# Performance work log

Measured on AMD Instinct MI355X. Metric: run time of the kernel, lower is better.

The kernel has to match this reference:

```python
import jax, jax.numpy as jnp
import numpy as np

NUM_CLASS = 20
STRIDE = 4.0
B, H, W, G, NV = 8, 128, 128, 64, 40


def setup_inputs() -> dict:
    key = jax.random.key(0)
    ks = jax.random.split(key, 8)
    keypoints = jax.random.normal(ks[0], (B, H, W, NUM_CLASS), jnp.float32)
    preg = jax.random.uniform(ks[1], (B, H, W, 4), jnp.float32, 1.0, 40.0)
    fpn = jax.random.normal(ks[2], (B, H, W, NUM_CLASS), jnp.float32)
    masks = jnp.ones((B, H, W, G), jnp.float32)
    scalar_y = jax.random.uniform(ks[3], (B, G), jnp.float32, 5.0, 25.0)
    scalar_x = jax.random.uniform(ks[4], (B, G), jnp.float32, 5.0, 25.0)
    # ground truth: [cy, cx, y1, x1, y2, x2, class]; rows >= NV are zero padding
    rng = np.random.default_rng(0)
    gt = np.zeros((B, G, 7), np.float32)
    cy = rng.uniform(20.0, 492.0, (B, NV)).astype(np.float32)
    cx = rng.uniform(20.0, 492.0, (B, NV)).astype(np.float32)
    hh = rng.uniform(16.0, 120.0, (B, NV)).astype(np.float32)
    ww = rng.uniform(16.0, 120.0, (B, NV)).astype(np.float32)
    gt[:, :NV, 0] = cy
    gt[:, :NV, 1] = cx
    gt[:, :NV, 2] = np.clip(cy - hh / 2, 1.0, 510.0)
    gt[:, :NV, 3] = np.clip(cx - ww / 2, 1.0, 510.0)
    gt[:, :NV, 4] = np.clip(cy + hh / 2, 1.0, 510.0)
    gt[:, :NV, 5] = np.clip(cx + ww / 2, 1.0, 510.0)
    gt[:, :NV, 6] = rng.integers(1, NUM_CLASS + 1, (B, NV)).astype(np.float32)
    return {
        "keypoints": keypoints,
        "preg": preg,
        "fpn": fpn,
        "ground_truth": jnp.asarray(gt),
        "masks": masks,
        "scalar_y": scalar_y,
        "scalar_x": scalar_x,
    }


def _image_loss(gravity_pred, dist_pred, heatmap_pred, gt, masks, sy, sx):
    f32 = jnp.float32
    Hh, Ww, C = gravity_pred.shape
    Gg = gt.shape[0]
    # padding boundary: first row whose cy (col 0) is the minimum (==0 padding)
    slice_index = jnp.argmin(gt[:, 0])
    valid = jnp.arange(Gg) < slice_index
    vf = valid.astype(f32)

    gy = (gt[:, 0] + 0.5) / STRIDE
    gx = (gt[:, 1] + 0.5) / STRIDE
    by1 = (gt[:, 2] + 0.5) / STRIDE
    bx1 = (gt[:, 3] + 0.5) / STRIDE
    by2 = (gt[:, 4] + 0.5) / STRIDE
    bx2 = (gt[:, 5] + 0.5) / STRIDE
    cid = gt[:, 6].astype(jnp.int32) - 1
    kp_y = jnp.clip(jnp.floor(gt[:, 0] / STRIDE).astype(jnp.int32), 0, Hh - 1)
    kp_x = jnp.clip(jnp.floor(gt[:, 1] / STRIDE).astype(jnp.int32), 0, Ww - 1)

    grid_y = (jnp.arange(Hh, dtype=f32) + 0.5)[:, None, None]  # [H,1,1]
    grid_x = (jnp.arange(Ww, dtype=f32) + 0.5)[None, :, None]  # [1,W,1]

    dist_l = grid_x - bx1  # [1,W,G]
    dist_r = bx2 - grid_x
    dist_t = grid_y - by1  # [H,1,G]
    dist_b = by2 - grid_y
    ymask = (dist_t > 0.0).astype(f32) * (dist_b > 0.0).astype(f32)
    xmask = (dist_l > 0.0).astype(f32) * (dist_r > 0.0).astype(f32)
    heatmask = ymask * xmask * masks * vf  # [H,W,G]
    dist_l = dist_l * heatmask
    dist_r = dist_r * heatmask
    dist_t = dist_t * heatmask
    dist_b = dist_b * heatmask
    loc = jnp.max(heatmask, axis=-1)  # [H,W]
    dist_area = (dist_l + dist_r) * (dist_t + dist_b)
    area_pad = dist_area + (1.0 - heatmask) * 1e8
    area_min = jnp.min(area_pad, axis=-1, keepdims=True)
    dist_mask = (dist_area == area_min).astype(f32) * loc[..., None]  # [H,W,G]
    dl = jnp.max(dist_l * dist_mask, axis=-1)
    dr = jnp.max(dist_r * dist_mask, axis=-1)
    dt = jnp.max(dist_t * dist_mask, axis=-1)
    db = jnp.max(dist_b * dist_mask, axis=-1)

    pl, pr, pt, pb = (dist_pred[..., k] for k in range(4))
    inter = (jnp.minimum(dl, pl) + jnp.minimum(dr, pr)) * (jnp.minimum(dt, pt) + jnp.minimum(db, pb))
    union = (dl + dr) * (dt + db) + (pl + pr) * (pt + pb) - inter
    iou = inter / (union + 1e-12)

    red = jnp.exp(-(((grid_y - 0.5 - jnp.floor(gy)) / jnp.sqrt(sy)) ** 2
                    + ((grid_x - 0.5 - jnp.floor(gx)) / jnp.sqrt(sx)) ** 2) / 2.0) * vf  # [H,W,G]
    iou_red = jnp.max(red, axis=-1)
    iou_loss = jnp.sum(-jnp.log(iou + 1e-12) * loc * (iou_red * 4.0 + 1.0))

    # per-class max over gts of that class (== boolean_mask + reduce_max; empty -> 0)
    seg = jnp.where(valid & (cid >= 0) & (cid < C), cid, C)
    red_gt = jnp.maximum(jax.ops.segment_max(red.transpose(2, 0, 1), seg, num_segments=C + 1)[:C], 0.0).transpose(1, 2, 0)
    hm_gt = jnp.maximum(jax.ops.segment_max(dist_mask.transpose(2, 0, 1), seg, num_segments=C + 1)[:C], 0.0).transpose(1, 2, 0)
    gt_kp = jnp.zeros((Hh, Ww, C + 1), f32).at[kp_y, kp_x, seg].max(vf)[..., :C]

    sig, ls = jax.nn.sigmoid, jax.nn.log_sigmoid
    pos = -(1.0 - sig(gravity_pred)) ** 2 * ls(gravity_pred) * gt_kp
    neg = -(1.0 - red_gt) ** 4 * sig(gravity_pred) ** 2 * (-gravity_pred + ls(gravity_pred)) * (1.0 - gt_kp)
    gravity_loss = jnp.sum(pos) + jnp.sum(neg)

    hpos = -10.0 * (1.0 - sig(heatmap_pred)) ** 2 * ls(heatmap_pred) * hm_gt
    hneg = -10.0 * sig(heatmap_pred) ** 2 * (-heatmap_pred + ls(heatmap_pred)) * (1.0 - hm_gt)
    s_hg = jnp.sum(hm_gt)
    hm_loss = jnp.sum(hneg) / (jnp.asarray(Hh * Ww * C, f32) - s_hg)

    cond = s_hg != 0.0
    safe_hg = jnp.where(cond, s_hg, 1.0)
    s_loc = jnp.sum(loc)
    safe_loc = jnp.where(s_loc > 0.0, s_loc, 1.0)
    n_valid = jnp.maximum(slice_index.astype(f32), 1.0)
    hm2 = hm_loss + jnp.sum(hpos) / safe_hg
    iou_out = jnp.where(cond, iou_loss / safe_loc, 0.0)
    grav_out = jnp.where(cond, gravity_loss / n_valid, 0.0)
    hm_out = jnp.where(cond, hm2, hm_loss)
    total = jnp.where(cond, iou_out + grav_out + hm2, hm_loss)
    return iou_out, hm_out, grav_out, total


def reference(keypoints, preg, fpn, ground_truth, masks, scalar_y, scalar_x):
    losses = jax.vmap(_image_loss)(keypoints, preg, fpn, ground_truth, masks, scalar_y, scalar_x)
    # layer returns the mean total loss over the batch
    return jnp.mean(losses[3])
```

## Files before the change

kernel.cpp:

```cpp
#include <hip/hip_runtime.h>
#include <math.h>

#define Bc 8
#define Hc 128
#define Wc 128
#define Cc 20
#define Gc 64
#define HWc (Hc*Wc)
#define NBLK (Bc*HWc/256)


__device__ __forceinline__ float wave_sum(float v) {
  #pragma unroll
  for (int o = 32; o > 0; o >>= 1) v += __shfl_down(v, o, 64);
  return v;
}

__global__ __launch_bounds__(256, 2) void main_kernel(
    const float* __restrict__ kpt, const float* __restrict__ preg,
    const float* __restrict__ fpn, const float* __restrict__ masks,
    const float* __restrict__ gt,  const float* __restrict__ sy,
    const float* __restrict__ sx,  float* __restrict__ ws)
{
  __shared__ float s_kpt[Cc*256];
  __shared__ float s_fpn[Cc*256];
  __shared__ float s_masks[16*256];
  __shared__ float4 s_red[Gc];
  __shared__ int s_kpix[Gc];
  __shared__ int s_seg[Gc];
  __shared__ int s_starts[Cc+2];
  __shared__ int s_counts[Cc+1];
  __shared__ int s_offs[Cc+1];
  __shared__ int s_nslice;
  __shared__ float s_part[4][6];

  const int T = threadIdx.x;
  const int b = blockIdx.x >> 6;
  const int pixbase = blockIdx.x * 256;
  const int pix = pixbase + T;
  const int hw = pix & (HWc-1);
  const int h = hw >> 7, w = hw & (Wc-1);

  const float4* __restrict__ kg4 = (const float4*)(kpt + (size_t)pixbase*Cc);
  const float4* __restrict__ fg4 = (const float4*)(fpn + (size_t)pixbase*Cc);
  const float4* __restrict__ mg4 = (const float4*)(masks + (size_t)pixbase*Gc);
  float4 kpr[5], fpr[5], mpr[4];
  #pragma unroll
  for (int k = 0; k < 5; ++k) { kpr[k] = kg4[T + 256*k]; fpr[k] = fg4[T + 256*k]; }
  #pragma unroll
  for (int k = 0; k < 4; ++k) mpr[k] = mg4[((T>>2) + 64*k)*16 + (T&3)];

  if (T < Cc+1) { s_counts[T] = 0; s_offs[T] = 0; }
  float cy = 0.f, cx = 0.f; int cls = Cc; bool valid = false;
  if (T < 64) {
    const float* grow = gt + (size_t)(b*Gc + T)*7;
    cy = grow[0]; cx = grow[1];
    float v = cy; int idx = T;
    #pragma unroll
    for (int o = 32; o > 0; o >>= 1) {
      const float ov = __shfl_down(v, o, 64);
      const int   oi = __shfl_down(idx, o, 64);
      if (ov < v || (ov == v && oi < idx)) { v = ov; idx = oi; }
    }
    const int slice = __shfl(idx, 0, 64);
    const int cid = (int)grow[6] - 1;
    cls = (cid >= 0 && cid < Cc) ? cid : Cc;
    valid = T < slice;
    s_seg[T] = (valid && cls < Cc) ? cls : Cc;
    if (T == 0) s_nslice = slice;
  }
  __syncthreads();
  if (T < 64 && valid) atomicAdd(&s_counts[cls], 1);
  __syncthreads();
  if (T == 0) {
    int acc = 0;
    #pragma unroll
    for (int c = 0; c < Cc+1; ++c) { s_starts[c] = acc; acc += s_counts[c]; }
    s_starts[Cc+1] = acc;
  }
  __syncthreads();
  if (T < 64 && valid) {
    const int pos = s_starts[cls] + atomicAdd(&s_offs[cls], 1);
    float4 rp;
    rp.x = floorf((cy + 0.5f)*0.25f);
    rp.y = floorf((cx + 0.5f)*0.25f);
    rp.z = 0.5f / sy[b*Gc + T];
    rp.w = 0.5f / sx[b*Gc + T];
    s_red[pos] = rp;
    int kpy = (int)floorf(cy*0.25f); kpy = kpy < 0 ? 0 : (kpy > Hc-1 ? Hc-1 : kpy);
    int kpx = (int)floorf(cx*0.25f); kpx = kpx < 0 ? 0 : (kpx > Wc-1 ? Wc-1 : kpx);
    s_kpix[pos] = kpy*Wc + kpx;
  }

  #pragma unroll
  for (int k = 0; k < 5; ++k) {
    const int base = (T + 256*k)*4;
    const float ke[4] = {kpr[k].x, kpr[k].y, kpr[k].z, kpr[k].w};
    const float fe[4] = {fpr[k].x, fpr[k].y, fpr[k].z, fpr[k].w};
    #pragma unroll
    for (int i = 0; i < 4; ++i) {
      const int li = base + i;
      const int p = li / 20;
      const int c = li - p*20;
      s_kpt[c*256 + p] = ke[i];
      s_fpn[c*256 + p] = fe[i];
    }
  }
  #pragma unroll
  for (int k = 0; k < 4; ++k) {
    const int p  = (T>>2) + 64*k;
    const int g0 = (T&3)*4;
    const float me[4] = {mpr[k].x, mpr[k].y, mpr[k].z, mpr[k].w};
    #pragma unroll
    for (int i = 0; i < 4; ++i) s_masks[(g0+i)*256 + p] = me[i];
  }
  #pragma unroll
  for (int k = 0; k < 4; ++k) mpr[k] = mg4[((T>>2) + 64*k)*16 + 4 + (T&3)];
  __syncthreads();

  const int nslice = s_nslice;
  const int nch = (nslice + 15) >> 4;

  const float wx = w + 0.5f, hy = h + 0.5f;
  const float wxp = wx - 0.125f, wxm = 0.125f - wx;
  const float hyp = hy - 0.125f, hym = 0.125f - hy;
  const float px_ = (float)w, py_ = (float)h;

  float amin = 3.0e38f, loc = 0.f, mmin = 0.f; int gmin = 0;
  for (int cc = 0; cc < nch; ++cc) {
    const int rem = nslice - cc*16;
    const int gend = rem < 16 ? rem : 16;
    for (int gl = 0; gl < gend; ++gl) {
      const int g = cc*16 + gl;
      const float* grow = gt + (size_t)(b*Gc + g)*7;
      const float m = s_masks[gl*256 + T];
      const float dl = fmaf(-0.25f, grow[3], wxp);
      const float dr = fmaf( 0.25f, grow[5], wxm);
      const float dt = fmaf(-0.25f, grow[2], hyp);
      const float db = fmaf( 0.25f, grow[4], hym);
      const bool inb = (dl > 0.f) & (dr > 0.f) & (dt > 0.f) & (db > 0.f);
      const float hm = inb ? m : 0.f;
      const float area = (dl*hm + dr*hm) * (dt*hm + db*hm);
      const float ap = area + (1.f - hm)*1e8f;
      if (ap < amin) { amin = ap; gmin = g; mmin = m; }
      loc = fmaxf(loc, hm);
    }
    if (cc + 1 < nch) {
      __syncthreads();
      #pragma unroll
      for (int k = 0; k < 4; ++k) {
        const int p  = (T>>2) + 64*k;
        const int g0 = (T&3)*4;
        const float me[4] = {mpr[k].x, mpr[k].y, mpr[k].z, mpr[k].w};
        #pragma unroll
        for (int i = 0; i < 4; ++i) s_masks[(g0+i)*256 + p] = me[i];
      }
      if (cc + 2 < nch) {
        #pragma unroll
        for (int k = 0; k < 4; ++k)
          mpr[k] = mg4[((T>>2) + 64*k)*16 + (cc+2)*4 + (T&3)];
      }
      __syncthreads();
    }
  }

  float dlm=0.f, drm=0.f, dtm=0.f, dbm=0.f, hmval=0.f; int cmin = Cc;
  if (loc > 0.f) {
    const float* gr = gt + (size_t)(b*Gc + gmin)*7;
    const float dl = fmaf(-0.25f, gr[3], wxp);
    const float dr = fmaf( 0.25f, gr[5], wxm);
    const float dt = fmaf(-0.25f, gr[2], hyp);
    const float db = fmaf( 0.25f, gr[4], hym);
    const float area = (dl*mmin + dr*mmin) * (dt*mmin + db*mmin);
    if (area == amin) {
      dlm = dl*mmin*loc; drm = dr*mmin*loc; dtm = dt*mmin*loc; dbm = db*mmin*loc;
      cmin = s_seg[gmin];
      hmval = loc;
    }
  }

  float gargmax = -1e30f, grav = 0.f, hneg = 0.f;
  int sb = s_starts[0];
  for (int c = 0; c < Cc; ++c) {
    const int s1 = s_starts[c+1];
    float ramax = -1e30f; bool kpv = false;
    for (int i = sb; i < s1; ++i) {
      const float4 rp = s_red[i];
      const int kpix = s_kpix[i];
      const float dy = py_ - rp.x, dx = px_ - rp.y;
      const float arg = -(dy*dy*rp.z + dx*dx*rp.w);
      ramax = fmaxf(ramax, arg);
      kpv = kpv | (kpix == hw);
    }
    sb = s1;
    const float rmax = __expf(ramax);
    gargmax = fmaxf(gargmax, ramax);

    const float x  = s_kpt[c*256 + T];
    const float e  = __expf(-fabsf(x));
    const float t  = 1.f + e;
    const float r  = 1.f / t;
    const float Lt = __logf(t);
    const float s  = (x >= 0.f) ? r : e*r;
    const float lsx = fminf(x, 0.f) - Lt;
    const float kv = kpv ? 1.f : 0.f;
    const float om = 1.f - rmax;
    const float om4 = (om*om)*(om*om);
    const float oms = 1.f - s;
    grav += (-(oms*oms)*lsx)*kv + (-om4*(s*s)*(lsx - x))*(1.f - kv);

    const float fx  = s_fpn[c*256 + T];
    const float ef  = __expf(-fabsf(fx));
    const float tf  = 1.f + ef;
    const float rf  = 1.f / tf;
    const float Lf  = __logf(tf);
    const float sf  = (fx >= 0.f) ? rf : ef*rf;
    const float lsf = fminf(fx, 0.f) - Lf;
    hneg += -10.f*(sf*sf)*(lsf - fx);
  }
  {
    const int e20 = s_starts[Cc+1];
    for (int i = sb; i < e20; ++i) {
      const float4 rp = s_red[i];
      const float dy = py_ - rp.x, dx = px_ - rp.y;
      gargmax = fmaxf(gargmax, -(dy*dy*rp.z + dx*dx*rp.w));
    }
  }
  const float iou_red = __expf(gargmax);

  const float4 p4 = *(const float4*)(preg + (size_t)pix*4);
  const float inter = (fminf(dlm,p4.x)+fminf(drm,p4.y)) * (fminf(dtm,p4.z)+fminf(dbm,p4.w));
  const float uni = (dlm+drm)*(dtm+dbm) + (p4.x+p4.y)*(p4.z+p4.w) - inter;
  const float iou = inter / (uni + 1e-12f);
  const float t_iou = -__logf(iou + 1e-12f) * loc * (iou_red*4.f + 1.f);

  float hpos = 0.f, shg = 0.f;
  if (hmval > 0.f && cmin < Cc) {
    const float fx  = s_fpn[cmin*256 + T];
    const float ef  = __expf(-fabsf(fx));
    const float tf  = 1.f + ef;
    const float rf  = 1.f / tf;
    const float Lf  = __logf(tf);
    const float sf  = (fx >= 0.f) ? rf : ef*rf;
    const float lsf = fminf(fx, 0.f) - Lf;
    const float osf = 1.f - sf;
    hpos = -10.f*(osf*osf)*lsf*hmval;
    hneg -= (-10.f*(sf*sf)*(lsf - fx))*hmval;
    shg = hmval;
  }

  float v0 = wave_sum(t_iou);
  float v1 = wave_sum(loc);
  float v2 = wave_sum(grav);
  float v3 = wave_sum(hpos);
  float v4 = wave_sum(hneg);
  float v5 = wave_sum(shg);
  const int wv = T >> 6, ln = T & 63;
  if (ln == 0) {
    s_part[wv][0]=v0; s_part[wv][1]=v1; s_part[wv][2]=v2;
    s_part[wv][3]=v3; s_part[wv][4]=v4; s_part[wv][5]=v5;
  }
  __syncthreads();
  if (T < 6)
    ws[(size_t)blockIdx.x*8 + T] =
        s_part[0][T] + s_part[1][T] + s_part[2][T] + s_part[3][T];
}

__global__ __launch_bounds__(256) void fin_kernel(
    const float* __restrict__ gt, const float* __restrict__ ws,
    float* __restrict__ out)
{
  const int T = threadIdx.x, wv = T >> 6, ln = T & 63;
  __shared__ float s_tot[Bc];
  #pragma unroll
  for (int rep = 0; rep < 2; ++rep) {
    const int b = wv + 4*rep;
    const float cy = gt[(size_t)(b*Gc + ln)*7];
    float v = cy; int idx = ln;
    #pragma unroll
    for (int o = 32; o > 0; o >>= 1) {
      const float ov = __shfl_down(v, o, 64);
      const int   oi = __shfl_down(idx, o, 64);
      if (ov < v || (ov == v && oi < idx)) { v = ov; idx = oi; }
    }
    const int slice = __shfl(idx, 0, 64);
    const float* pb = ws + (size_t)(b*64 + ln)*8;
    const float a0 = wave_sum(pb[0]);
    const float a1 = wave_sum(pb[1]);
    const float a2 = wave_sum(pb[2]);
    const float a3 = wave_sum(pb[3]);
    const float a4 = wave_sum(pb[4]);
    const float a5 = wave_sum(pb[5]);
    if (ln == 0) {
      const float nv       = fmaxf((float)slice, 1.0f);
      const float hm_loss  = a4 / ((float)(HWc*Cc) - a5);
      const bool  cond     = (a5 != 0.0f);
      const float safe_hg  = cond ? a5 : 1.0f;
      const float safe_loc = (a1 > 0.0f) ? a1 : 1.0f;
      const float hm2      = hm_loss + a3/safe_hg;
      s_tot[b] = cond ? (a0/safe_loc + a2/nv + hm2) : hm_loss;
    }
  }
  __syncthreads();
  if (T == 0) {
    float s = 0.f;
    #pragma unroll
    for (int i = 0; i < Bc; ++i) s += s_tot[i];
    out[0] = s * (1.0f/(float)Bc);
  }
}

extern "C" void kernel_launch(void* const* d_in, const int* in_sizes, int n_in,
                              void* d_out, int out_size, void* d_ws, size_t ws_size,
                              hipStream_t stream) {
  const float* kpt  = (const float*)d_in[0];
  const float* preg = (const float*)d_in[1];
  const float* fpn  = (const float*)d_in[2];
  const float* gt   = (const float*)d_in[3];
  const float* mk   = (const float*)d_in[4];
  const float* sy   = (const float*)d_in[5];
  const float* sx   = (const float*)d_in[6];
  float* ws  = (float*)d_ws;
  float* out = (float*)d_out;

  main_kernel<<<NBLK, 256, 0, stream>>>(kpt, preg, fpn, mk, gt, sy, sx, ws);
  fin_kernel<<<1, 256, 0, stream>>>(ws ? gt : gt, ws, out);
}
```

Baseline: 120.7 us.

## Load per-pixel rows directly into registers instead of LDS transpose staging

Each thread now loads its own 20 keypoint, 20 fpn and up to 64 mask values straight into registers as float4 rows, replacing the coalesced loads that were transposed through shared memory. This removes about 60KB of LDS per block, the chunked mask double-buffering and several __syncthreads, and merges the gt setup into one wave-local pass. Mask loads are skipped beyond the valid-box count, and the class loop is fully unrolled. The trade-off is uncoalesced strided global loads and much higher register pressure (mrow[16] and two 5-element float4 rows).

After: 122.8 us. Within noise of the previous version (+1.7%).

```diff
diff --git a/kernel.cpp b/kernel.cpp
--- a/kernel.cpp
+++ b/kernel.cpp
@@ -22,104 +22,76 @@
     const float* __restrict__ gt,  const float* __restrict__ sy,
     const float* __restrict__ sx,  float* __restrict__ ws)
 {
-  __shared__ float s_kpt[Cc*256];
-  __shared__ float s_fpn[Cc*256];
-  __shared__ float s_masks[16*256];
   __shared__ float4 s_red[Gc];
   __shared__ int s_kpix[Gc];
   __shared__ int s_seg[Gc];
   __shared__ int s_starts[Cc+2];
   __shared__ int s_counts[Cc+1];
   __shared__ int s_offs[Cc+1];
-  __shared__ int s_nslice;
   __shared__ float s_part[4][6];
 
-  const int T = threadIdx.x;
+  const int T = threadIdx.x, ln = T & 63;
   const int b = blockIdx.x >> 6;
-  const int pixbase = blockIdx.x * 256;
-  const int pix = pixbase + T;
+  const int pix = blockIdx.x*256 + T;
   const int hw = pix & (HWc-1);
   const int h = hw >> 7, w = hw & (Wc-1);
-
-  const float4* __restrict__ kg4 = (const float4*)(kpt + (size_t)pixbase*Cc);
-  const float4* __restrict__ fg4 = (const float4*)(fpn + (size_t)pixbase*Cc);
-  const float4* __restrict__ mg4 = (const float4*)(masks + (size_t)pixbase*Gc);
-  float4 kpr[5], fpr[5], mpr[4];
-  #pragma unroll
-  for (int k = 0; k < 5; ++k) { kpr[k] = kg4[T + 256*k]; fpr[k] = fg4[T + 256*k]; }
-  #pragma unroll
-  for (int k = 0; k < 4; ++k) mpr[k] = mg4[((T>>2) + 64*k)*16 + (T&3)];
-
-  if (T < Cc+1) { s_counts[T] = 0; s_offs[T] = 0; }
-  float cy = 0.f, cx = 0.f; int cls = Cc; bool valid = false;
+  const float* gtb = gt + (size_t)b*Gc*7;
+
+  const float cy_l = gtb[ln*7];
+
+  const float4* __restrict__ kq4 = (const float4*)(kpt + (size_t)pix*Cc);
+  const float4* __restrict__ fq4 = (const float4*)(fpn + (size_t)pix*Cc);
+  float4 krow[5], frow[5];
+  #pragma unroll
+  for (int k = 0; k < 5; ++k) { krow[k] = kq4[k]; frow[k] = fq4[k]; }
+  const float4 p4 = *(const float4*)(preg + (size_t)pix*4);
+
+  float v = cy_l; int idx = ln;
+  #pragma unroll
+  for (int o = 32; o > 0; o >>= 1) {
+    const float ov = __shfl_down(v, o, 64);
+    const int   oi = __shfl_down(idx, o, 64);
+    if (ov < v || (ov == v && oi < idx)) { v = ov; idx = oi; }
+  }
+  const int nslice = __shfl(idx, 0, 64);
+
+  const float4* __restrict__ mg4 = (const float4*)(masks + (size_t)pix*Gc);
+  float4 mrow[16];
+  #pragma unroll
+  for (int k = 0; k < 16; ++k) {
+    mrow[k] = make_float4(0.f, 0.f, 0.f, 0.f);
+    if (k*4 < nslice) mrow[k] = mg4[k];
+  }
+
   if (T < 64) {
-    const float* grow = gt + (size_t)(b*Gc + T)*7;
-    cy = grow[0]; cx = grow[1];
-    float v = cy; int idx = T;
-    #pragma unroll
-    for (int o = 32; o > 0; o >>= 1) {
-      const float ov = __shfl_down(v, o, 64);
-      const int   oi = __shfl_down(idx, o, 64);
-      if (ov < v || (ov == v && oi < idx)) { v = ov; idx = oi; }
-    }
-    const int slice = __shfl(idx, 0, 64);
-    const int cid = (int)grow[6] - 1;
-    cls = (cid >= 0 && cid < Cc) ? cid : Cc;
-    valid = T < slice;
+    if (T < Cc+1) { s_counts[T] = 0; s_offs[T] = 0; }
+    const int cid = (int)gtb[T*7+6] - 1;
+    const int cls = (cid >= 0 && cid < Cc) ? cid : Cc;
+    const bool valid = T < nslice;
     s_seg[T] = (valid && cls < Cc) ? cls : Cc;
-    if (T == 0) s_nslice = slice;
+    if (valid) atomicAdd(&s_counts[cls], 1);
+    if (T == 0) {
+      int acc = 0;
+      #pragma unroll
+      for (int c = 0; c < Cc+1; ++c) { s_starts[c] = acc; acc += s_counts[c]; }
+      s_starts[Cc+1] = acc;
+    }
+    if (valid) {
+      const int pos = s_starts[cls] + atomicAdd(&s_offs[cls], 1);
+      const float cyv = cy_l;
+      const float cxv = gtb[T*7+1];
+      float4 rp;
+      rp.x = floorf((cyv + 0.5f)*0.25f);
+      rp.y = floorf((cxv + 0.5f)*0.25f);
+      rp.z = 0.5f / sy[b*Gc + T];
+      rp.w = 0.5f / sx[b*Gc + T];
+      s_red[pos] = rp;
+      int kpy = (int)floorf(cyv*0.25f); kpy = kpy < 0 ? 0 : (kpy > Hc-1 ? Hc-1 : kpy);
+      int kpx = (int)floorf(cxv*0.25f); kpx = kpx < 0 ? 0 : (kpx > Wc-1 ? Wc-1 : kpx);
+      s_kpix[pos] = kpy*Wc + kpx;
+    }
   }
   __syncthreads();
-  if (T < 64 && valid) atomicAdd(&s_counts[cls], 1);
-  __syncthreads();
-  if (T == 0) {
-    int acc = 0;
-    #pragma unroll
-    for (int c = 0; c < Cc+1; ++c) { s_starts[c] = acc; acc += s_counts[c]; }
-    s_starts[Cc+1] = acc;
-  }
-  __syncthreads();
-  if (T < 64 && valid) {
-    const int pos = s_starts[cls] + atomicAdd(&s_offs[cls], 1);
-    float4 rp;
-    rp.x = floorf((cy + 0.5f)*0.25f);
-    rp.y = floorf((cx + 0.5f)*0.25f);
-    rp.z = 0.5f / sy[b*Gc + T];
-    rp.w = 0.5f / sx[b*Gc + T];
-    s_red[pos] = rp;
-    int kpy = (int)floorf(cy*0.25f); kpy = kpy < 0 ? 0 : (kpy > Hc-1 ? Hc-1 : kpy);
-    int kpx = (int)floorf(cx*0.25f); kpx = kpx < 0 ? 0 : (kpx > Wc-1 ? Wc-1 : kpx);
-    s_kpix[pos] = kpy*Wc + kpx;
-  }
-
-  #pragma unroll
-  for (int k = 0; k < 5; ++k) {
-    const int base = (T + 256*k)*4;
-    const float ke[4] = {kpr[k].x, kpr[k].y, kpr[k].z, kpr[k].w};
-    const float fe[4] = {fpr[k].x, fpr[k].y, fpr[k].z, fpr[k].w};
-    #pragma unroll
-    for (int i = 0; i < 4; ++i) {
-      const int li = base + i;
-      const int p = li / 20;
-      const int c = li - p*20;
-      s_kpt[c*256 + p] = ke[i];
-      s_fpn[c*256 + p] = fe[i];
-    }
-  }
-  #pragma unroll
-  for (int k = 0; k < 4; ++k) {
-    const int p  = (T>>2) + 64*k;
-    const int g0 = (T&3)*4;
-    const float me[4] = {mpr[k].x, mpr[k].y, mpr[k].z, mpr[k].w};
-    #pragma unroll
-    for (int i = 0; i < 4; ++i) s_masks[(g0+i)*256 + p] = me[i];
-  }
-  #pragma unroll
-  for (int k = 0; k < 4; ++k) mpr[k] = mg4[((T>>2) + 64*k)*16 + 4 + (T&3)];
-  __syncthreads();
-
-  const int nslice = s_nslice;
-  const int nch = (nslice + 15) >> 4;
 
   const float wx = w + 0.5f, hy = h + 0.5f;
   const float wxp = wx - 0.125f, wxm = 0.125f - wx;
@@ -127,46 +99,33 @@
   const float px_ = (float)w, py_ = (float)h;
 
   float amin = 3.0e38f, loc = 0.f, mmin = 0.f; int gmin = 0;
-  for (int cc = 0; cc < nch; ++cc) {
-    const int rem = nslice - cc*16;
-    const int gend = rem < 16 ? rem : 16;
-    for (int gl = 0; gl < gend; ++gl) {
-      const int g = cc*16 + gl;
-      const float* grow = gt + (size_t)(b*Gc + g)*7;
-      const float m = s_masks[gl*256 + T];
-      const float dl = fmaf(-0.25f, grow[3], wxp);
-      const float dr = fmaf( 0.25f, grow[5], wxm);
-      const float dt = fmaf(-0.25f, grow[2], hyp);
-      const float db = fmaf( 0.25f, grow[4], hym);
-      const bool inb = (dl > 0.f) & (dr > 0.f) & (dt > 0.f) & (db > 0.f);
-      const float hm = inb ? m : 0.f;
-      const float area = (dl*hm + dr*hm) * (dt*hm + db*hm);
-      const float ap = area + (1.f - hm)*1e8f;
-      if (ap < amin) { amin = ap; gmin = g; mmin = m; }
-      loc = fmaxf(loc, hm);
-    }
-    if (cc + 1 < nch) {
-      __syncthreads();
+  #pragma unroll
+  for (int c16 = 0; c16 < 4; ++c16) {
+    if (c16*16 < nslice) {
       #pragma unroll
-      for (int k = 0; k < 4; ++k) {
-        const int p  = (T>>2) + 64*k;
-        const int g0 = (T&3)*4;
-        const float me[4] = {mpr[k].x, mpr[k].y, mpr[k].z, mpr[k].w};
-        #pragma unroll
-        for (int i = 0; i < 4; ++i) s_masks[(g0+i)*256 + p] = me[i];
+      for (int j = 0; j < 16; ++j) {
+        const int g = c16*16 + j;
+        const float4 mq = mrow[g>>2];
+        const float m = ((g&3)==0) ? mq.x : ((g&3)==1) ? mq.y
+                      : ((g&3)==2) ? mq.z : mq.w;
+        const float dl = fmaf(-0.25f, gtb[g*7+3], wxp);
+        const float dr = fmaf( 0.25f, gtb[g*7+5], wxm);
+        const float dt = fmaf(-0.25f, gtb[g*7+2], hyp);
+        const float db = fmaf( 0.25f, gtb[g*7+4], hym);
+        const bool inb = (dl > 0.f) & (dr > 0.f) & (dt > 0.f) & (db > 0.f)
+                         & (g < nslice);
+        const float hm = inb ? m : 0.f;
+        const float area = (dl*hm + dr*hm) * (dt*hm + db*hm);
+        const float ap = area + (1.f - hm)*1e8f;
+        if (ap < amin) { amin = ap; gmin = g; mmin = m; }
+        loc = fmaxf(loc, hm);
       }
-      if (cc + 2 < nch) {
-        #pragma unroll
-        for (int k = 0; k < 4; ++k)
-          mpr[k] = mg4[((T>>2) + 64*k)*16 + (cc+2)*4 + (T&3)];
-      }
-      __syncthreads();
     }
   }
 
   float dlm=0.f, drm=0.f, dtm=0.f, dbm=0.f, hmval=0.f; int cmin = Cc;
   if (loc > 0.f) {
-    const float* gr = gt + (size_t)(b*Gc + gmin)*7;
+    const float* gr = gtb + gmin*7;
     const float dl = fmaf(-0.25f, gr[3], wxp);
     const float dr = fmaf( 0.25f, gr[5], wxm);
     const float dt = fmaf(-0.25f, gr[2], hyp);
@@ -181,6 +140,7 @@
 
   float gargmax = -1e30f, grav = 0.f, hneg = 0.f;
   int sb = s_starts[0];
+  #pragma unroll
   for (int c = 0; c < Cc; ++c) {
     const int s1 = s_starts[c+1];
     float ramax = -1e30f; bool kpv = false;
@@ -196,7 +156,9 @@
     const float rmax = __expf(ramax);
     gargmax = fmaxf(gargmax, ramax);
 
-    const float x  = s_kpt[c*256 + T];
+    const float4 kq = krow[c>>2];
+    const float x  = ((c&3)==0) ? kq.x : ((c&3)==1) ? kq.y
+                   : ((c&3)==2) ? kq.z : kq.w;
     const float e  = __expf(-fabsf(x));
     const float t  = 1.f + e;
     const float r  = 1.f / t;
@@ -209,7 +171,9 @@
     const float oms = 1.f - s;
     grav += (-(oms*oms)*lsx)*kv + (-om4*(s*s)*(lsx - x))*(1.f - kv);
 
-    const float fx  = s_fpn[c*256 + T];
+    const float4 fq = frow[c>>2];
+    const float fx  = ((c&3)==0) ? fq.x : ((c&3)==1) ? fq.y
+                    : ((c&3)==2) ? fq.z : fq.w;
     const float ef  = __expf(-fabsf(fx));
     const float tf  = 1.f + ef;
     const float rf  = 1.f / tf;
@@ -228,7 +192,6 @@
   }
   const float iou_red = __expf(gargmax);
 
-  const float4 p4 = *(const float4*)(preg + (size_t)pix*4);
   const float inter = (fminf(dlm,p4.x)+fminf(drm,p4.y)) * (fminf(dtm,p4.z)+fminf(dbm,p4.w));
   const float uni = (dlm+drm)*(dtm+dbm) + (p4.x+p4.y)*(p4.z+p4.w) - inter;
   const float iou = inter / (uni + 1e-12f);
@@ -236,7 +199,7 @@
 
   float hpos = 0.f, shg = 0.f;
   if (hmval > 0.f && cmin < Cc) {
-    const float fx  = s_fpn[cmin*256 + T];
+    const float fx  = fpn[(size_t)pix*Cc + cmin];
     const float ef  = __expf(-fabsf(fx));
     const float tf  = 1.f + ef;
     const float rf  = 1.f / tf;
@@ -255,7 +218,7 @@
   float v3 = wave_sum(hpos);
   float v4 = wave_sum(hneg);
   float v5 = wave_sum(shg);
-  const int wv = T >> 6, ln = T & 63;
+  const int wv = T >> 6;
   if (ln == 0) {
     s_part[wv][0]=v0; s_part[wv][1]=v1; s_part[wv][2]=v2;
     s_part[wv][3]=v3; s_part[wv][4]=v4; s_part[wv][5]=v5;
@@ -324,5 +287,5 @@
   float* out = (float*)d_out;
 
   main_kernel<<<NBLK, 256, 0, stream>>>(kpt, preg, fpn, mk, gt, sy, sx, ws);
-  fin_kernel<<<1, 256, 0, stream>>>(ws ? gt : gt, ws, out);
-}
+  fin_kernel<<<1, 256, 0, stream>>>(gt, ws, out);
+}
```
